# Kernel optimization log

Measured on AMD Instinct MI355X. Metric: run time of the kernel, lower is better.

The kernel has to match this reference:

```python
import jax, jax.numpy as jnp
from jax import lax
import numpy as np

# Model dims (see shape_source)
D_MODEL = 768
N_LAYERS = 8
D_STATE = 16
EXPAND = 2
D_INNER = EXPAND * D_MODEL          # 1536
DT_RANK = (D_MODEL + 15) // 16       # 48
D_CONV = 4
PATCH = 16
IMG = 224
CH = 3
BATCH = 8


def rmsnorm(x, w, eps=1e-5):
    return x * lax.rsqrt(jnp.mean(x * x, axis=-1, keepdims=True) + eps) * w


def patch_embed(img, w, b):
    # img: [B,C,H,W] -> tokens [B, N, d_model]
    x = lax.conv_general_dilated(img, w, (PATCH, PATCH), 'VALID',
                                 dimension_numbers=('NCHW', 'OIHW', 'NCHW'))
    x = x + b[None, :, None, None]
    Bsz = img.shape[0]
    return x.reshape(Bsz, D_MODEL, -1).transpose(0, 2, 1)


def mamba_block(x, in_w, cw, cb, xw, dtw, dtb, a_log, d_p, ow):
    # x: [B, L, d_model]
    Bsz, L, _ = x.shape
    xz = x @ in_w.T                                   # [B,L,2*ED]
    xin, z = jnp.split(xz, 2, axis=-1)
    # causal depthwise conv over L
    xc = lax.conv_general_dilated(xin.transpose(0, 2, 1), cw, (1,),
                                  [(D_CONV - 1, 0)],
                                  dimension_numbers=('NCH', 'OIH', 'NCH'),
                                  feature_group_count=D_INNER)
    xin = jax.nn.silu((xc + cb[None, :, None]).transpose(0, 2, 1))  # [B,L,ED]
    dbc = xin @ xw.T                                  # [B,L,dt_rank+2N]
    delta, Bm, Cm = jnp.split(dbc, [DT_RANK, DT_RANK + D_STATE], axis=-1)
    delta = jax.nn.softplus(delta @ dtw.T + dtb)      # [B,L,ED]
    A = -jnp.exp(a_log)                               # [ED,N]
    dA = jnp.exp(delta[..., None] * A)                # [B,L,ED,N]
    dBx = (delta * xin)[..., None] * Bm[:, :, None, :]  # [B,L,ED,N]

    def step(h, inp):
        a, bx = inp
        h = a * h + bx
        return h, h

    h0 = jnp.zeros((Bsz, D_INNER, D_STATE), x.dtype)
    _, hs = lax.scan(step, h0, (dA.transpose(1, 0, 2, 3), dBx.transpose(1, 0, 2, 3)))
    y = jnp.einsum('lben,bln->ble', hs, Cm)           # [B,L,ED]
    y = y + d_p * xin
    y = y * jax.nn.silu(z)
    return y @ ow.T                                   # [B,L,d_model]


def setup_inputs() -> dict:
    key = jax.random.key(0)
    ks = jax.random.split(key, 16)
    s = 0.02
    nl = N_LAYERS
    inp = {
        'rgb': jax.random.normal(ks[0], (BATCH, CH, IMG, IMG), jnp.float32),
        't': jax.random.normal(ks[1], (BATCH, CH, IMG, IMG), jnp.float32),
        'pe_w': jax.random.normal(ks[2], (D_MODEL, CH, PATCH, PATCH), jnp.float32) * s,
        'pe_b': jnp.zeros((D_MODEL,), jnp.float32),
        'in_proj_w': jax.random.normal(ks[3], (nl, 2 * D_INNER, D_MODEL), jnp.float32) * s,
        'conv_w': jax.random.normal(ks[4], (nl, D_INNER, 1, D_CONV), jnp.float32) * s,
        'conv_b': jnp.zeros((nl, D_INNER), jnp.float32),
        'x_proj_w': jax.random.normal(ks[5], (nl, DT_RANK + 2 * D_STATE, D_INNER), jnp.float32) * s,
        'dt_proj_w': jax.random.normal(ks[6], (nl, D_INNER, DT_RANK), jnp.float32) * s,
        'dt_proj_b': jax.random.normal(ks[7], (nl, D_INNER), jnp.float32) * s,
        'A_log': jnp.log(jnp.broadcast_to(jnp.arange(1.0, D_STATE + 1.0), (nl, D_INNER, D_STATE))),
        'D': jnp.ones((nl, D_INNER), jnp.float32),
        'out_proj_w': jax.random.normal(ks[8], (nl, D_MODEL, D_INNER), jnp.float32) * s,
        'norm_w': jnp.ones((nl, D_MODEL), jnp.float32),
    }
    return inp


def reference(rgb, t, pe_w, pe_b, in_proj_w, conv_w, conv_b, x_proj_w,
              dt_proj_w, dt_proj_b, A_log, D, out_proj_w, norm_w):
    rt = patch_embed(rgb, pe_w, pe_b)   # [B,196,768]
    tt = patch_embed(t, pe_w, pe_b)
    x = jnp.concatenate([rt, tt], axis=1)  # [B,392,768]
    for i in range(N_LAYERS):
        x = x + mamba_block(rmsnorm(x, norm_w[i]), in_proj_w[i], conv_w[i],
                            conv_b[i], x_proj_w[i], dt_proj_w[i], dt_proj_b[i],
                            A_log[i], D[i], out_proj_w[i])
    Bsz = rgb.shape[0]
    # [B,2N,D] -> [B,2N,D,1] -> transpose(0,3) -> [1,2N,D,B] -> [2B,C,H,W]
    out = jnp.transpose(x[..., None], (3, 1, 2, 0)).reshape(2 * Bsz, CH, IMG, IMG)
    return out[:Bsz], out[Bsz:]
```

## Files before the change

### kernel.cpp

```cpp
#include <hip/hip_runtime.h>
#include <cstddef>
#include <cstdint>

#define L_TOK 392
#define BATCH 8
#define DM    768
#define ED    1536
#define NST   16
#define DTR   48
#define ROWS  (BATCH * L_TOK)

#define C_CH 8
#define CLEN 49
#define EGB  24

#define XP_Z  6


typedef unsigned short ushortT;
typedef __bf16 bf16x8 __attribute__((ext_vector_type(8)));
typedef unsigned short us8 __attribute__((ext_vector_type(8)));
typedef unsigned short us4 __attribute__((ext_vector_type(4)));
typedef float f32x4 __attribute__((ext_vector_type(4)));

#define LOG2E 1.4426950408889634f

__device__ __forceinline__ float bf2f(ushortT u) {
    union { unsigned int i; float f; } v; v.i = ((unsigned int)u) << 16; return v.f;
}
__device__ __forceinline__ ushortT f2bf(float f) {
    union { float f; unsigned int i; } v; v.f = f;
    unsigned int r = v.i + 0x7FFFu + ((v.i >> 16) & 1u);
    return (ushortT)(r >> 16);
}

__device__ __forceinline__ void gload16(const void* g, void* l) {
    __builtin_amdgcn_global_load_lds(
        (const __attribute__((address_space(1))) void*)g,
        (__attribute__((address_space(3))) void*)l, 16, 0, 0);
}

enum { EPI_STORE = 0, EPI_BIAS = 1, EPI_BIAS_SOFTPLUS = 2, EPI_ADD = 3 };

#define INW_F4 (2 * ED * DM / 4)
#define XW_F4  (80 * ED / 4)
#define OW_F4  (DM * ED / 4)
#define PE_F4  (DM * DM / 4)

__global__ __launch_bounds__(256)
void convert3_kernel(const float* __restrict__ s0, ushortT* __restrict__ d0, int n0,
                     const float* __restrict__ s1, ushortT* __restrict__ d1, int n1,
                     const float* __restrict__ s2, ushortT* __restrict__ d2, int n2)
{
    int idx = blockIdx.x * 256 + threadIdx.x;
    const float* s; ushortT* d;
    if (idx < n0) { s = s0; d = d0; }
    else if (idx < n0 + n1) { idx -= n0; s = s1; d = d1; }
    else if (idx < n0 + n1 + n2) { idx -= n0 + n1; s = s2; d = d2; }
    else return;
    float4 f = *(const float4*)(s + (size_t)idx * 4);
    us4 h; h.x = f2bf(f.x); h.y = f2bf(f.y); h.z = f2bf(f.z); h.w = f2bf(f.w);
    *(us4*)(d + (size_t)idx * 4) = h;
}

template <int EPI, bool C_BF, bool SPLIT, bool ATOMIC, bool PARTIAL>
__global__ __launch_bounds__(256)
void gemm_mfma(const ushortT* __restrict__ A, int lda,
               const ushortT* __restrict__ W, int ldw,
               const float* __restrict__ bias,
               void* __restrict__ Cv, void* __restrict__ Cv2, int ldc,
               int M, int N, int K, int kchunk)
{
    __shared__ ushortT As[2][128 * 32];
    __shared__ ushortT Ws[2][128 * 32];

    const int tid  = threadIdx.x;
    const int lane = tid & 63;
    const int wave = tid >> 6;
    const int wm   = wave >> 1;
    const int wn   = wave & 1;
    const int quad = lane >> 4;
    const int l16  = lane & 15;

    const int gx   = gridDim.x;
    const int nwg  = gx * gridDim.y;
    const int flat = blockIdx.y * gx + blockIdx.x;
    const int q = nwg >> 3, r = nwg & 7;
    const int xcd = flat & 7, sidx = flat >> 3;
    const int swz = (xcd < r ? xcd * (q + 1) : r * (q + 1) + (xcd - r) * q) + sidx;

    const int m0 = (swz / gx) * 128;
    const int n0 = (swz % gx) * 128;
    const int kb = blockIdx.z * kchunk;
    const int KT = kchunk / 32;

    const int srow = lane >> 2;
    const int scol = (lane & 3) * 8;
    const ushortT* aBase = A + (size_t)(m0 + srow) * lda + scol;
    const ushortT* wBase = W + (size_t)(n0 + srow) * ldw + scol;

    auto stage = [&](int buf, int k0) {
#pragma unroll
        for (int c = 0; c < 2; ++c) {
            const int seg = wave * 2 + c;
            gload16(aBase + (size_t)(seg * 16) * lda + k0, &As[buf][seg * 512]);
            gload16(wBase + (size_t)(seg * 16) * ldw + k0, &Ws[buf][seg * 512]);
        }
    };

    f32x4 acc[4][4] = {};

    auto compute = [&](int buf) {
        bf16x8 af[4], bw[4];
#pragma unroll
        for (int t = 0; t < 4; ++t) {
            us8 ta = *(const us8*)&As[buf][(wm * 64 + t * 16 + l16) * 32 + quad * 8];
            af[t] = __builtin_bit_cast(bf16x8, ta);
            us8 tb = *(const us8*)&Ws[buf][(wn * 64 + t * 16 + l16) * 32 + quad * 8];
            bw[t] = __builtin_bit_cast(bf16x8, tb);
        }
#pragma unroll
        for (int i = 0; i < 4; ++i)
#pragma unroll
            for (int j = 0; j < 4; ++j)
                acc[i][j] = __builtin_amdgcn_mfma_f32_16x16x32_bf16(
                    af[i], bw[j], acc[i][j], 0, 0, 0);
    };

    stage(0, kb);
    __syncthreads();

    for (int kt = 0; kt < KT; ++kt) {
        if (kt + 1 < KT) stage((kt & 1) ^ 1, kb + (kt + 1) * 32);
        compute(kt & 1);
        __syncthreads();
    }

#pragma unroll
    for (int i = 0; i < 4; ++i) {
#pragma unroll
        for (int r2 = 0; r2 < 4; ++r2) {
            int gm = m0 + wm * 64 + i * 16 + quad * 4 + r2;
            if (gm >= M) continue;
#pragma unroll
            for (int j = 0; j < 4; ++j) {
                int gn = n0 + wn * 64 + j * 16 + l16;
                if (gn >= N) continue;
                float v = acc[i][j][r2];
                if (EPI == EPI_BIAS) v += bias[gn];
                void* dst = Cv;
                int cn = gn;
                if (SPLIT && gn >= ED) { dst = Cv2; cn = gn - ED; }
                size_t off = (size_t)gm * ldc + cn;
                if (PARTIAL) {
                    ((float*)dst)[(size_t)blockIdx.z * M * ldc + off] = v;
                } else if (ATOMIC) {
                    atomicAdd((float*)dst + off, v);
                } else if (C_BF) {
                    ((ushortT*)dst)[off] = f2bf(v);
                } else {
                    float* p = (float*)dst + off;
                    *p = (EPI == EPI_ADD) ? v + *p : v;
                }
            }
        }
    }
}

__global__ __launch_bounds__(256)
void reduce_partials_kernel(const float* __restrict__ P, float* __restrict__ dbc)
{
    int idx = blockIdx.x * 256 + threadIdx.x;
    if (idx >= ROWS * 80) return;
    float s = 0.f;
#pragma unroll
    for (int z = 0; z < XP_Z; ++z)
        s += P[(size_t)z * ROWS * 80 + idx];
    dbc[idx] = s;
}

template <int EPI, bool A_BF, bool C_BF>
__global__ __launch_bounds__(256)
void gemm_nt(const void* __restrict__ Av, int lda,
             const float* __restrict__ W, int ldw,
             const float* __restrict__ bias,
             void* __restrict__ Cv, int ldc,
             int M, int N, int K)
{
    __shared__ float As[16][68];
    __shared__ float Bs[16][68];
    const int tid = threadIdx.x;
    const int tx  = tid & 15;
    const int ty  = tid >> 4;
    const int bm  = blockIdx.y * 64;
    const int bn  = blockIdx.x * 64;
    const int lr  = tid >> 2;
    const int lk  = (tid & 3) * 4;

    float acc[4][4] = {};

    for (int k0 = 0; k0 < K; k0 += 16) {
        float a0 = 0.f, a1 = 0.f, a2 = 0.f, a3 = 0.f;
        float w0 = 0.f, w1 = 0.f, w2 = 0.f, w3 = 0.f;
        int ga = bm + lr;
        if (ga < M) {
            if (A_BF) {
                const ushortT* A = (const ushortT*)Av;
                ushort4 t = *(const ushort4*)(A + (size_t)ga * lda + k0 + lk);
                a0 = bf2f(t.x); a1 = bf2f(t.y); a2 = bf2f(t.z); a3 = bf2f(t.w);
            } else {
                const float* A = (const float*)Av;
                float4 t = *(const float4*)(A + (size_t)ga * lda + k0 + lk);
                a0 = t.x; a1 = t.y; a2 = t.z; a3 = t.w;
            }
        }
        int gw = bn + lr;
        if (gw < N) {
            float4 t = *(const float4*)(W + (size_t)gw * ldw + k0 + lk);
            w0 = t.x; w1 = t.y; w2 = t.z; w3 = t.w;
        }
        As[lk + 0][lr] = a0; As[lk + 1][lr] = a1;
        As[lk + 2][lr] = a2; As[lk + 3][lr] = a3;
        Bs[lk + 0][lr] = w0; Bs[lk + 1][lr] = w1;
        Bs[lk + 2][lr] = w2; Bs[lk + 3][lr] = w3;
        __syncthreads();
#pragma unroll
        for (int k = 0; k < 16; ++k) {
            float4 a4 = *(const float4*)&As[k][ty * 4];
            float4 b4 = *(const float4*)&Bs[k][tx * 4];
            float a[4] = {a4.x, a4.y, a4.z, a4.w};
            float b[4] = {b4.x, b4.y, b4.z, b4.w};
#pragma unroll
            for (int i = 0; i < 4; ++i)
#pragma unroll
                for (int j = 0; j < 4; ++j)
                    acc[i][j] += a[i] * b[j];
        }
        __syncthreads();
    }

#pragma unroll
    for (int i = 0; i < 4; ++i) {
        int gm = bm + ty * 4 + i;
        if (gm >= M) continue;
#pragma unroll
        for (int j = 0; j < 4; ++j) {
            int gn = bn + tx * 4 + j;
            if (gn >= N) continue;
            float v = acc[i][j];
            if (EPI == EPI_BIAS) v += bias[gn];
            if (EPI == EPI_BIAS_SOFTPLUS) {
                v += bias[gn];
                v = fmaxf(v, 0.f) + log1pf(expf(-fabsf(v)));
            }
            size_t off = (size_t)gm * ldc + gn;
            if (C_BF) {
                ((ushortT*)Cv)[off] = f2bf(v);
            } else {
                float* p = (float*)Cv + off;
                *p = (EPI == EPI_ADD) ? v + *p : v;
            }
        }
    }
}

__global__ __launch_bounds__(256)
void rmsnorm_kernel(const float* __restrict__ x, const float* __restrict__ w,
                    ushortT* __restrict__ xn)
{
    int r = blockIdx.x;
    const float* xr = x + (size_t)r * DM;
    float v[3];
    float s = 0.f;
#pragma unroll
    for (int i = 0; i < 3; ++i) {
        v[i] = xr[threadIdx.x + i * 256];
        s += v[i] * v[i];
    }
#pragma unroll
    for (int o = 32; o > 0; o >>= 1) s += __shfl_down(s, o, 64);
    __shared__ float wsum[4];
    __shared__ float scale_s;
    int wave = threadIdx.x >> 6;
    if ((threadIdx.x & 63) == 0) wsum[wave] = s;
    __syncthreads();
    if (threadIdx.x == 0) {
        float t = wsum[0] + wsum[1] + wsum[2] + wsum[3];
        scale_s = rsqrtf(t * (1.f / 768.f) + 1e-5f);
    }
    __syncthreads();
    float sc = scale_s;
#pragma unroll
    for (int i = 0; i < 3; ++i) {
        int d = threadIdx.x + i * 256;
        xn[(size_t)r * DM + d] = f2bf(v[i] * sc * w[d]);
    }
}

__global__ __launch_bounds__(256)
void conv_silu_kernel(const ushortT* __restrict__ xc, const float* __restrict__ cw,
                      const float* __restrict__ cb, ushortT* __restrict__ xin)
{
    int idx = blockIdx.x * 256 + threadIdx.x;
    if (idx >= ROWS * ED / 2) return;
    int e2 = (idx % (ED / 2)) * 2;
    int r  = idx / (ED / 2);
    int l  = r % L_TOK;
    const ushortT* base = xc + (size_t)r * ED + e2;
    ushort2 t0 = *(const ushort2*)(base);
    ushort2 t1 = {0, 0}, t2 = {0, 0}, t3 = {0, 0};
    if (l >= 1) t1 = *(const ushort2*)(base - ED);
    if (l >= 2) t2 = *(const ushort2*)(base - 2 * ED);
    if (l >= 3) t3 = *(const ushort2*)(base - 3 * ED);
    ushort2 out;
#pragma unroll
    for (int c = 0; c < 2; ++c) {
        int e = e2 + c;
        float acc = cb[e] + cw[e * 4 + 3] * bf2f(c ? t0.y : t0.x);
        acc += cw[e * 4 + 2] * bf2f(c ? t1.y : t1.x);
        acc += cw[e * 4 + 1] * bf2f(c ? t2.y : t2.x);
        acc += cw[e * 4 + 0] * bf2f(c ? t3.y : t3.x);
        ushortT o = f2bf(acc / (1.f + __expf(-acc)));
        if (c) out.y = o; else out.x = o;
    }
    *(ushort2*)(xin + (size_t)r * ED + e2) = out;
}

__global__ __launch_bounds__(64)
void scan_part1(const ushortT* __restrict__ delta, const ushortT* __restrict__ xin,
                const float* __restrict__ dbc, const float* __restrict__ a_log,
                float* __restrict__ hend, float* __restrict__ sdl)
{
    __shared__ float BsL[CLEN * 16];
    const int tid = threadIdx.x;
    const int bid = blockIdx.x;
    const int eg = bid % EGB;
    const int c  = (bid / EGB) % C_CH;
    const int b  = bid / (EGB * C_CH);
    const int e  = eg * 64 + tid;
    const int l0 = c * CLEN;
    const int rb = b * L_TOK + l0;

    for (int i = tid; i < CLEN * 16; i += 64) {
        int s = i >> 4, n = i & 15;
        BsL[i] = dbc[(size_t)(rb + s) * 80 + 48 + n];
    }
    __syncthreads();

    float a[16];
    const float* ar = a_log + (size_t)e * 16;
#pragma unroll
    for (int n = 0; n < 16; ++n) a[n] = -__expf(ar[n]) * LOG2E;

    float h[16];
#pragma unroll
    for (int n = 0; n < 16; ++n) h[n] = 0.f;
    float sum_dl = 0.f;

    const size_t base = (size_t)rb * ED + e;
    float rdl[7], rxi[7];
#pragma unroll
    for (int j = 0; j < 7; ++j) {
        rdl[j] = bf2f(delta[base + (size_t)j * ED]);
        rxi[j] = bf2f(xin[base + (size_t)j * ED]);
    }
    for (int s0 = 0; s0 < CLEN; s0 += 7) {
#pragma unroll
        for (int j = 0; j < 7; ++j) {
            const int s = s0 + j;
            float dl = rdl[j], xi = rxi[j];
            int sp = s + 7; if (sp > CLEN - 1) sp = CLEN - 1;
            rdl[j] = bf2f(delta[base + (size_t)sp * ED]);
            rxi[j] = bf2f(xin[base + (size_t)sp * ED]);
            float dlxi = dl * xi;
            sum_dl += dl;
#pragma unroll
            for (int n = 0; n < 16; ++n)
                h[n] = __builtin_amdgcn_exp2f(dl * a[n]) * h[n] + dlxi * BsL[s * 16 + n];
        }
    }

    float* hp = hend + (((size_t)b * ED + e) * C_CH + c) * 16;
#pragma unroll
    for (int n = 0; n < 16; ++n) hp[n] = h[n];
    sdl[((size_t)b * ED + e) * C_CH + c] = sum_dl;
}

__global__ __launch_bounds__(64)
void scan_part2(const ushortT* __restrict__ delta, const ushortT* __restrict__ xin,
                const float* __restrict__ dbc, const ushortT* __restrict__ zb,
                const float* __restrict__ a_log, const float* __restrict__ dvec,
                const float* __restrict__ hend, const float* __restrict__ sdl,
                ushortT* __restrict__ y)
{
    __shared__ float BsL[CLEN * 16];
    __shared__ float CsL[CLEN * 16];
    const int tid = threadIdx.x;
    const int bid = blockIdx.x;
    const int eg = bid % EGB;
    const int c  = (bid / EGB) % C_CH;
    const int b  = bid / (EGB * C_CH);
    const int e  = eg * 64 + tid;
    const int l0 = c * CLEN;
    const int rb = b * L_TOK + l0;

    for (int i = tid; i < CLEN * 16; i += 64) {
        int s = i >> 4, n = i & 15;
        size_t row = (size_t)(rb + s) * 80;
        BsL[i] = dbc[row + 48 + n];
        CsL[i] = dbc[row + 64 + n];
    }
    __syncthreads();

    float a[16];
    const float* ar = a_log + (size_t)e * 16;
#pragma unroll
    for (int n = 0; n < 16; ++n) a[n] = -__expf(ar[n]) * LOG2E;
    const float dcf = dvec[e];

    float h[16];
#pragma unroll
    for (int n = 0; n < 16; ++n) h[n] = 0.f;
    const float* hb = hend + (((size_t)b * ED + e) * C_CH) * 16;
    const float* sb = sdl + ((size_t)b * ED + e) * C_CH;
    for (int cc = 0; cc < c; ++cc) {
        float sv = sb[cc];
#pragma unroll
        for (int n = 0; n < 16; ++n)
            h[n] = __builtin_amdgcn_exp2f(a[n] * sv) * h[n] + hb[cc * 16 + n];
    }

    const size_t base = (size_t)rb * ED + e;
    float rdl[7], rxi[7], rz[7];
#pragma unroll
    for (int j = 0; j < 7; ++j) {
        rdl[j] = bf2f(delta[base + (size_t)j * ED]);
        rxi[j] = bf2f(xin[base + (size_t)j * ED]);
        rz[j]  = bf2f(zb[base + (size_t)j * ED]);
    }
    for (int s0 = 0; s0 < CLEN; s0 += 7) {
#pragma unroll
        for (int j = 0; j < 7; ++j) {
            const int s = s0 + j;
            float dl = rdl[j], xi = rxi[j], z = rz[j];
            int sp = s + 7; if (sp > CLEN - 1) sp = CLEN - 1;
            rdl[j] = bf2f(delta[base + (size_t)sp * ED]);
            rxi[j] = bf2f(xin[base + (size_t)sp * ED]);
            rz[j]  = bf2f(zb[base + (size_t)sp * ED]);
            float dlxi = dl * xi;
            float yv = 0.f;
#pragma unroll
            for (int n = 0; n < 16; ++n) {
                h[n] = __builtin_amdgcn_exp2f(dl * a[n]) * h[n] + dlxi * BsL[s * 16 + n];
                yv += h[n] * CsL[s * 16 + n];
            }
            yv += dcf * xi;
            float sz = z / (1.f + __expf(-z));
            y[base + (size_t)s * ED] = f2bf(yv * sz);
        }
    }
}

__global__ __launch_bounds__(256)
void im2col_kernel(const float* __restrict__ rgb, const float* __restrict__ timg,
                   ushortT* __restrict__ P,
                   const float* __restrict__ pe_w, ushortT* __restrict__ peb)
{
    int idx = blockIdx.x * 256 + threadIdx.x;
    if (idx < ROWS * DM) {
        int k = idx % DM;
        int r = idx / DM;
        int b = r / L_TOK;
        int l = r % L_TOK;
        const float* img = (l < 196) ? rgb : timg;
        int p  = (l < 196) ? l : l - 196;
        int py = p / 14, px = p % 14;
        int c  = k >> 8;
        int ph = (k >> 4) & 15;
        int pw = k & 15;
        P[idx] = f2bf(img[(((size_t)b * 3 + c) * 224 + (py * 16 + ph)) * 224 + (px * 16 + pw)]);
        return;
    }
    int u = idx - ROWS * DM;
    if (u < PE_F4) {
        float4 f = *(const float4*)(pe_w + (size_t)u * 4);
        us4 h; h.x = f2bf(f.x); h.y = f2bf(f.y); h.z = f2bf(f.z); h.w = f2bf(f.w);
        *(us4*)(peb + (size_t)u * 4) = h;
    }
}

__global__ __launch_bounds__(256)
void out_transpose_kernel(const float* __restrict__ x, float* __restrict__ out)
{
    int idx = blockIdx.x * 256 + threadIdx.x;
    if (idx >= ROWS * DM) return;
    int b = idx & 7;
    int d = (idx >> 3) % DM;
    int l = idx / (8 * DM);
    out[idx] = x[((size_t)(b * L_TOK + l)) * DM + d];
}

extern "C" void kernel_launch(void* const* d_in, const int* in_sizes, int n_in,
                              void* d_out, int out_size, void* d_ws, size_t ws_size,
                              hipStream_t stream)
{
    (void)in_sizes; (void)n_in; (void)out_size; (void)ws_size;

    const float* rgb  = (const float*)d_in[0];
    const float* timg = (const float*)d_in[1];
    const float* pe_w = (const float*)d_in[2];
    const float* pe_b = (const float*)d_in[3];
    const float* in_w = (const float*)d_in[4];
    const float* cw   = (const float*)d_in[5];
    const float* cb   = (const float*)d_in[6];
    const float* xw   = (const float*)d_in[7];
    const float* dtw  = (const float*)d_in[8];
    const float* dtb  = (const float*)d_in[9];
    const float* alog = (const float*)d_in[10];
    const float* dvec = (const float*)d_in[11];
    const float* ow   = (const float*)d_in[12];
    const float* nw   = (const float*)d_in[13];

    char* p = (char*)d_ws;
    float*   X   = (float*)p;    p += (size_t)ROWS * DM * 4;
    ushortT* XC  = (ushortT*)p;  p += (size_t)ROWS * ED * 2;
    ushortT* Zb  = (ushortT*)p;  p += (size_t)ROWS * ED * 2;
    ushortT* XIN = (ushortT*)p;  p += (size_t)ROWS * ED * 2;
    ushortT* DEL = (ushortT*)p;  p += (size_t)ROWS * ED * 2;
    float*   DBC = (float*)p;    p += (size_t)ROWS * 80 * 4;
    ushortT* XN  = DEL;

    ushortT* INWB = XIN;
    ushortT* XWB  = (ushortT*)DBC;
    ushortT* PEB  = Zb;

    float* POUT = (float*)d_out;
    float* HEND = (float*)d_out;
    float* SDL  = HEND + (size_t)BATCH * ED * C_CH * 16;
    ushortT* OWB = (ushortT*)((char*)d_out +
                   ((size_t)BATCH * ED * C_CH * 16 + (size_t)BATCH * ED * C_CH) * 4);

    dim3 b256(256);
    const int MT = (ROWS + 127) / 128;
    const int SCAN_BLOCKS = BATCH * C_CH * EGB;
    const int CVT_BLOCKS = (INW_F4 + XW_F4 + OW_F4 + 255) / 256;

    im2col_kernel<<<(ROWS * DM + PE_F4 + 255) / 256, b256, 0, stream>>>(
        rgb, timg, XC, pe_w, PEB);
    gemm_mfma<EPI_BIAS, false, false, false, false><<<dim3(DM / 128, MT), b256, 0, stream>>>(
        XC, DM, PEB, DM, pe_b, X, nullptr, DM, ROWS, DM, DM, DM);

    for (int i = 0; i < 8; ++i) {
        const float* in_wi = in_w + (size_t)i * 2 * ED * DM;
        const float* cwi   = cw   + (size_t)i * ED * 4;
        const float* cbi   = cb   + (size_t)i * ED;
        const float* xwi   = xw   + (size_t)i * 80 * ED;
        const float* dtwi  = dtw  + (size_t)i * ED * DTR;
        const float* dtbi  = dtb  + (size_t)i * ED;
        const float* ali   = alog + (size_t)i * ED * NST;
        const float* dvi   = dvec + (size_t)i * ED;
        const float* owi   = ow   + (size_t)i * DM * ED;
        const float* nwi   = nw   + (size_t)i * DM;

        convert3_kernel<<<CVT_BLOCKS, b256, 0, stream>>>(
            in_wi, INWB, INW_F4, xwi, XWB, XW_F4, owi, OWB, OW_F4);
        rmsnorm_kernel<<<ROWS, b256, 0, stream>>>(X, nwi, XN);
        gemm_mfma<EPI_STORE, true, true, false, false><<<dim3(2 * ED / 128, MT), b256, 0, stream>>>(
            XN, DM, INWB, DM, nullptr, XC, Zb, ED, ROWS, 2 * ED, DM, DM);
        conv_silu_kernel<<<(ROWS * ED / 2 + 255) / 256, b256, 0, stream>>>(
            XC, cwi, cbi, XIN);
        gemm_mfma<EPI_STORE, false, false, false, true><<<dim3(1, MT, XP_Z), b256, 0, stream>>>(
            XIN, ED, XWB, ED, nullptr, POUT, nullptr, 80, ROWS, 80, ED, ED / XP_Z);
        reduce_partials_kernel<<<(ROWS * 80 + 255) / 256, b256, 0, stream>>>(
            POUT, DBC);
        gemm_nt<EPI_BIAS_SOFTPLUS, false, true><<<dim3(ED / 64, ROWS / 64), b256, 0, stream>>>(
            DBC, 80, dtwi, DTR, dtbi, DEL, ED, ROWS, ED, DTR);
        scan_part1<<<SCAN_BLOCKS, 64, 0, stream>>>(
            DEL, XIN, DBC, ali, HEND, SDL);
        scan_part2<<<SCAN_BLOCKS, 64, 0, stream>>>(
            DEL, XIN, DBC, Zb, ali, dvi, HEND, SDL, XC);
        gemm_mfma<EPI_ADD, false, false, true, false><<<dim3(DM / 128, MT, 2), b256, 0, stream>>>(
            XC, ED, OWB, ED, nullptr, X, nullptr, DM, ROWS, DM, ED, ED / 2);
    }

    out_transpose_kernel<<<(ROWS * DM + 255) / 256, b256, 0, stream>>>(
        X, (float*)d_out);
}
```

Before: 1.630 ms.

## Fuse two-pass chunked selective scan into one kernel with shared-memory carry

Merges the two scan passes into a single kernel. Each 128-thread block handles 16 channels across all 8 chunks of one batch, and chunk end states and delta sums are exchanged through shared memory instead of global buffers. This removes one launch per layer and the global round-trip of the chunk states. The cost is lower parallelism: 768 blocks of 128 threads with 16-lane channel groups, so global loads of delta, xin and z are less coalesced. C is also stored in shared memory as bf16, which adds rounding error.

```diff
diff --git a/kernel.cpp b/kernel.cpp
--- a/kernel.cpp
+++ b/kernel.cpp
@@ -12,7 +12,6 @@
 
 #define C_CH 8
 #define CLEN 49
-#define EGB  24
 
 #define XP_Z  6
 
@@ -326,24 +325,36 @@
     *(ushort2*)(xin + (size_t)r * ED + e2) = out;
 }
 
-__global__ __launch_bounds__(64)
-void scan_part1(const ushortT* __restrict__ delta, const ushortT* __restrict__ xin,
-                const float* __restrict__ dbc, const float* __restrict__ a_log,
-                float* __restrict__ hend, float* __restrict__ sdl)
-{
-    __shared__ float BsL[CLEN * 16];
+__global__ __launch_bounds__(128)
+void scan_fused(const ushortT* __restrict__ delta, const ushortT* __restrict__ xin,
+                const float* __restrict__ dbc, const ushortT* __restrict__ zb,
+                const float* __restrict__ a_log, const float* __restrict__ dvec,
+                ushortT* __restrict__ y)
+{
+    __shared__ float  BsL[L_TOK * 16];
+    __shared__ ushortT CsL[L_TOK * 16];
+    __shared__ float  HsL[C_CH][16][16];
+    __shared__ float  SdL[C_CH][16];
+
     const int tid = threadIdx.x;
+    const int el  = tid & 15;
+    const int c   = tid >> 4;
     const int bid = blockIdx.x;
-    const int eg = bid % EGB;
-    const int c  = (bid / EGB) % C_CH;
-    const int b  = bid / (EGB * C_CH);
-    const int e  = eg * 64 + tid;
-    const int l0 = c * CLEN;
-    const int rb = b * L_TOK + l0;
-
-    for (int i = tid; i < CLEN * 16; i += 64) {
-        int s = i >> 4, n = i & 15;
-        BsL[i] = dbc[(size_t)(rb + s) * 80 + 48 + n];
+    const int eg  = bid % 96;
+    const int b   = bid / 96;
+    const int e   = eg * 16 + el;
+    const int rb  = b * L_TOK;
+    const int l0  = c * CLEN;
+
+    for (int i4 = tid; i4 < L_TOK * 4; i4 += 128) {
+        int s = i4 >> 2, n4 = (i4 & 3) * 4;
+        size_t row = (size_t)(rb + s) * 80;
+        float4 fb = *(const float4*)(dbc + row + 48 + n4);
+        *(f32x4*)&BsL[s * 16 + n4] = (f32x4){fb.x, fb.y, fb.z, fb.w};
+        float4 fc = *(const float4*)(dbc + row + 64 + n4);
+        us4 hc; hc.x = f2bf(fc.x); hc.y = f2bf(fc.y);
+        hc.z = f2bf(fc.z); hc.w = f2bf(fc.w);
+        *(us4*)&CsL[s * 16 + n4] = hc;
     }
     __syncthreads();
 
@@ -352,85 +363,52 @@
 #pragma unroll
     for (int n = 0; n < 16; ++n) a[n] = -__expf(ar[n]) * LOG2E;
 
+    const size_t base = (size_t)(rb + l0) * ED + e;
+
+    {
+        float h[16];
+#pragma unroll
+        for (int n = 0; n < 16; ++n) h[n] = 0.f;
+        float sum_dl = 0.f;
+        float rdl[7], rxi[7];
+#pragma unroll
+        for (int j = 0; j < 7; ++j) {
+            rdl[j] = bf2f(delta[base + (size_t)j * ED]);
+            rxi[j] = bf2f(xin[base + (size_t)j * ED]);
+        }
+        for (int s0 = 0; s0 < CLEN; s0 += 7) {
+#pragma unroll
+            for (int j = 0; j < 7; ++j) {
+                const int s = s0 + j;
+                float dl = rdl[j], xi = rxi[j];
+                int sp = s + 7; if (sp > CLEN - 1) sp = CLEN - 1;
+                rdl[j] = bf2f(delta[base + (size_t)sp * ED]);
+                rxi[j] = bf2f(xin[base + (size_t)sp * ED]);
+                float dlxi = dl * xi;
+                sum_dl += dl;
+#pragma unroll
+                for (int n = 0; n < 16; ++n)
+                    h[n] = __builtin_amdgcn_exp2f(dl * a[n]) * h[n]
+                         + dlxi * BsL[(l0 + s) * 16 + n];
+            }
+        }
+#pragma unroll
+        for (int n = 0; n < 16; ++n) HsL[c][n][el] = h[n];
+        SdL[c][el] = sum_dl;
+    }
+    __syncthreads();
+
     float h[16];
 #pragma unroll
     for (int n = 0; n < 16; ++n) h[n] = 0.f;
-    float sum_dl = 0.f;
-
-    const size_t base = (size_t)rb * ED + e;
-    float rdl[7], rxi[7];
-#pragma unroll
-    for (int j = 0; j < 7; ++j) {
-        rdl[j] = bf2f(delta[base + (size_t)j * ED]);
-        rxi[j] = bf2f(xin[base + (size_t)j * ED]);
-    }
-    for (int s0 = 0; s0 < CLEN; s0 += 7) {
-#pragma unroll
-        for (int j = 0; j < 7; ++j) {
-            const int s = s0 + j;
-            float dl = rdl[j], xi = rxi[j];
-            int sp = s + 7; if (sp > CLEN - 1) sp = CLEN - 1;
-            rdl[j] = bf2f(delta[base + (size_t)sp * ED]);
-            rxi[j] = bf2f(xin[base + (size_t)sp * ED]);
-            float dlxi = dl * xi;
-            sum_dl += dl;
-#pragma unroll
-            for (int n = 0; n < 16; ++n)
-                h[n] = __builtin_amdgcn_exp2f(dl * a[n]) * h[n] + dlxi * BsL[s * 16 + n];
-        }
-    }
-
-    float* hp = hend + (((size_t)b * ED + e) * C_CH + c) * 16;
-#pragma unroll
-    for (int n = 0; n < 16; ++n) hp[n] = h[n];
-    sdl[((size_t)b * ED + e) * C_CH + c] = sum_dl;
-}
-
-__global__ __launch_bounds__(64)
-void scan_part2(const ushortT* __restrict__ delta, const ushortT* __restrict__ xin,
-                const float* __restrict__ dbc, const ushortT* __restrict__ zb,
-                const float* __restrict__ a_log, const float* __restrict__ dvec,
-                const float* __restrict__ hend, const float* __restrict__ sdl,
-                ushortT* __restrict__ y)
-{
-    __shared__ float BsL[CLEN * 16];
-    __shared__ float CsL[CLEN * 16];
-    const int tid = threadIdx.x;
-    const int bid = blockIdx.x;
-    const int eg = bid % EGB;
-    const int c  = (bid / EGB) % C_CH;
-    const int b  = bid / (EGB * C_CH);
-    const int e  = eg * 64 + tid;
-    const int l0 = c * CLEN;
-    const int rb = b * L_TOK + l0;
-
-    for (int i = tid; i < CLEN * 16; i += 64) {
-        int s = i >> 4, n = i & 15;
-        size_t row = (size_t)(rb + s) * 80;
-        BsL[i] = dbc[row + 48 + n];
-        CsL[i] = dbc[row + 64 + n];
-    }
-    __syncthreads();
-
-    float a[16];
-    const float* ar = a_log + (size_t)e * 16;
-#pragma unroll
-    for (int n = 0; n < 16; ++n) a[n] = -__expf(ar[n]) * LOG2E;
+    for (int cc = 0; cc < c; ++cc) {
+        float sv = SdL[cc][el];
+#pragma unroll
+        for (int n = 0; n < 16; ++n)
+            h[n] = __builtin_amdgcn_exp2f(a[n] * sv) * h[n] + HsL[cc][n][el];
+    }
     const float dcf = dvec[e];
 
-    float h[16];
-#pragma unroll
-    for (int n = 0; n < 16; ++n) h[n] = 0.f;
-    const float* hb = hend + (((size_t)b * ED + e) * C_CH) * 16;
-    const float* sb = sdl + ((size_t)b * ED + e) * C_CH;
-    for (int cc = 0; cc < c; ++cc) {
-        float sv = sb[cc];
-#pragma unroll
-        for (int n = 0; n < 16; ++n)
-            h[n] = __builtin_amdgcn_exp2f(a[n] * sv) * h[n] + hb[cc * 16 + n];
-    }
-
-    const size_t base = (size_t)rb * ED + e;
     float rdl[7], rxi[7], rz[7];
 #pragma unroll
     for (int j = 0; j < 7; ++j) {
@@ -451,8 +429,9 @@
             float yv = 0.f;
 #pragma unroll
             for (int n = 0; n < 16; ++n) {
-                h[n] = __builtin_amdgcn_exp2f(dl * a[n]) * h[n] + dlxi * BsL[s * 16 + n];
-                yv += h[n] * CsL[s * 16 + n];
+                h[n] = __builtin_amdgcn_exp2f(dl * a[n]) * h[n]
+                     + dlxi * BsL[(l0 + s) * 16 + n];
+                yv += h[n] * bf2f(CsL[(l0 + s) * 16 + n]);
             }
             yv += dcf * xi;
             float sz = z / (1.f + __expf(-z));
@@ -535,15 +514,13 @@
     ushortT* PEB  = Zb;
 
     float* POUT = (float*)d_out;
-    float* HEND = (float*)d_out;
-    float* SDL  = HEND + (size_t)BATCH * ED * C_CH * 16;
     ushortT* OWB = (ushortT*)((char*)d_out +
                    ((size_t)BATCH * ED * C_CH * 16 + (size_t)BATCH * ED * C_CH) * 4);
 
     dim3 b256(256);
     const int MT = (ROWS + 127) / 128;
-    const int SCAN_BLOCKS = BATCH * C_CH * EGB;
     const int CVT_BLOCKS = (INW_F4 + XW_F4 + OW_F4 + 255) / 256;
+    const int SCAN_BLOCKS = BATCH * 96;
 
     im2col_kernel<<<(ROWS * DM + PE_F4 + 255) / 256, b256, 0, stream>>>(
         rgb, timg, XC, pe_w, PEB);
@@ -575,10 +552,8 @@
             POUT, DBC);
         gemm_nt<EPI_BIAS_SOFTPLUS, false, true><<<dim3(ED / 64, ROWS / 64), b256, 0, stream>>>(
             DBC, 80, dtwi, DTR, dtbi, DEL, ED, ROWS, ED, DTR);
-        scan_part1<<<SCAN_BLOCKS, 64, 0, stream>>>(
-            DEL, XIN, DBC, ali, HEND, SDL);
-        scan_part2<<<SCAN_BLOCKS, 64, 0, stream>>>(
-            DEL, XIN, DBC, Zb, ali, dvi, HEND, SDL, XC);
+        scan_fused<<<SCAN_BLOCKS, 128, 0, stream>>>(
+            DEL, XIN, DBC, Zb, ali, dvi, XC);
         gemm_mfma<EPI_ADD, false, false, true, false><<<dim3(DM / 128, MT, 2), b256, 0, stream>>>(
             XC, ED, OWB, ED, nullptr, X, nullptr, DM, ROWS, DM, ED, ED / 2);
     }
```

Result: slower. 2.006 ms (+23.0%).
